# Kernel tuning notes

Hardware: AMD Instinct MI355X
Metric: run time of the kernel (lower is better)

The kernel has to match this reference:

```python
import jax, jax.numpy as jnp
import numpy as np

B, T, C, H = 512, 40, 512, 512


def _gru_dir(x, Wih, Whh, bih, bhh):
    """Single-direction PyTorch-convention GRU. x: [B,T,C] -> [B,T,H]."""
    Hh = Whh.shape[1]
    # precompute input projections for all timesteps: [B,T,3H]
    gx = jnp.einsum('btc,gc->btg', x, Wih) + bih

    def step(h, gxt):
        gh = h @ Whh.T + bhh  # [B,3H]
        r = jax.nn.sigmoid(gxt[:, :Hh] + gh[:, :Hh])
        z = jax.nn.sigmoid(gxt[:, Hh:2 * Hh] + gh[:, Hh:2 * Hh])
        n = jnp.tanh(gxt[:, 2 * Hh:] + r * gh[:, 2 * Hh:])
        h_new = (1.0 - z) * n + z * h
        return h_new, h_new

    h0 = jnp.zeros((x.shape[0], Hh), x.dtype)
    _, ys = jax.lax.scan(step, h0, jnp.swapaxes(gx, 0, 1))  # [T,B,H]
    return jnp.swapaxes(ys, 0, 1)


def setup_inputs() -> dict:
    key = jax.random.key(0)
    ks = jax.random.split(key, 10)
    s = 1.0 / np.sqrt(H)  # PyTorch default init scale
    lengths = jax.random.randint(ks[0], (B,), 5, T + 1)
    valid = jnp.arange(T)[None, :] < lengths[:, None]  # [B,T]
    ref_expr = jax.random.normal(ks[1], (B, T, C), jnp.float32) * valid[..., None]
    mk = lambda k, shape: jax.random.uniform(k, shape, jnp.float32, -s, s)
    return {
        'ref_expr': ref_expr,
        'Wih_f': mk(ks[2], (3 * H, C)), 'Whh_f': mk(ks[3], (3 * H, H)),
        'bih_f': mk(ks[4], (3 * H,)), 'bhh_f': mk(ks[5], (3 * H,)),
        'Wih_b': mk(ks[6], (3 * H, C)), 'Whh_b': mk(ks[7], (3 * H, H)),
        'bih_b': mk(ks[8], (3 * H,)), 'bhh_b': mk(ks[9], (3 * H,)),
    }


def reference(ref_expr, Wih_f, Whh_f, bih_f, bhh_f, Wih_b, Whh_b, bih_b, bhh_b):
    # padded positions are all-zero embedding vectors -> masked out
    valid = jnp.any(ref_expr != 0, axis=-1)  # [B,T], True = keep
    y_fwd = _gru_dir(ref_expr, Wih_f, Whh_f, bih_f, bhh_f)
    y_bwd = _gru_dir(ref_expr[:, ::-1], Wih_b, Whh_b, bih_b, bhh_b)[:, ::-1]
    y_word = jnp.concatenate([y_fwd, y_bwd], axis=-1)  # [B,T,2H]
    # masked max pooling over valid tokens (output_type='max')
    neg = jnp.finfo(y_word.dtype).min
    y = jnp.max(jnp.where(valid[..., None], y_word, neg), axis=1, keepdims=True)
    return y  # [B,1,2H]
```

## Files before the change

### kernel.cpp

```cpp
#include <hip/hip_runtime.h>
#include <hip/hip_bf16.h>
#include <float.h>

#define BB 512
#define TT 40
#define CC 512
#define HH 512

typedef short bf16x8 __attribute__((ext_vector_type(8)));
typedef float f32x4 __attribute__((ext_vector_type(4)));
typedef unsigned short ushortx8 __attribute__((ext_vector_type(8)));

#define LDSH 49152
#define LDSF 98304
#define LDSTOT 98320

__device__ __forceinline__ unsigned short f2bf(float f){
  union { float f; unsigned int i; } v; v.f = f;
  unsigned int r = v.i + 0x7fffu + ((v.i >> 16) & 1u);
  return (unsigned short)(r >> 16);
}

__device__ __forceinline__ bf16x8 load_sc0(const unsigned short* p){
  bf16x8 r;
  asm volatile("global_load_dwordx4 %0, %1, off sc0" : "=v"(r) : "v"(p));
  return r;
}
#define WAITV(N) do { asm volatile("s_waitcnt vmcnt(" #N ")" ::: "memory"); \
                      __builtin_amdgcn_sched_barrier(0); } while(0)

__device__ __forceinline__ float fast_sigmoid(float x){
  return __builtin_amdgcn_rcpf(1.f + __expf(-x));
}
__device__ __forceinline__ float fast_tanh(float x){
  return 1.f - 2.f*__builtin_amdgcn_rcpf(__expf(2.f*x) + 1.f);
}

__global__ void prep_x_kernel(const float* __restrict__ x, unsigned short* __restrict__ xb,
                              float* __restrict__ maskT){
  int w = blockIdx.x*4 + (threadIdx.x>>6);
  int lane = threadIdx.x & 63;
  const float* src = x + (size_t)w*CC + lane*8;
  f32x4 a = *(const f32x4*)(src);
  f32x4 b = *(const f32x4*)(src+4);
  ushortx8 o;
  o[0]=f2bf(a[0]); o[1]=f2bf(a[1]); o[2]=f2bf(a[2]); o[3]=f2bf(a[3]);
  o[4]=f2bf(b[0]); o[5]=f2bf(b[1]); o[6]=f2bf(b[2]); o[7]=f2bf(b[3]);
  *(ushortx8*)(xb + (size_t)w*CC + lane*8) = o;
  bool nz = (a[0]!=0.f)||(a[1]!=0.f)||(a[2]!=0.f)||(a[3]!=0.f)||
            (b[0]!=0.f)||(b[1]!=0.f)||(b[2]!=0.f)||(b[3]!=0.f);
  unsigned long long bal = __ballot(nz);
  if (lane==0){
    int b_ = w / TT, t_ = w % TT;
    maskT[t_*BB + b_] = bal ? 1.0f : 0.0f;
  }
}

__global__ void cvt_kernel(const float* __restrict__ src, unsigned short* __restrict__ dst, int n8){
  int i = blockIdx.x*blockDim.x + threadIdx.x;
  if (i < n8){
    f32x4 a = *(const f32x4*)(src + i*8);
    f32x4 b = *(const f32x4*)(src + i*8 + 4);
    ushortx8 o;
    o[0]=f2bf(a[0]); o[1]=f2bf(a[1]); o[2]=f2bf(a[2]); o[3]=f2bf(a[3]);
    o[4]=f2bf(b[0]); o[5]=f2bf(b[1]); o[6]=f2bf(b[2]); o[7]=f2bf(b[3]);
    *(ushortx8*)(dst + i*8) = o;
  }
}

__global__ void init_h_kernel(unsigned short* __restrict__ hb, unsigned int* __restrict__ ctr){
  int i = blockIdx.x*blockDim.x + threadIdx.x;
  hb[i] = 0;
  if (i < 8) ctr[i*32] = 0u;
}

__global__ __launch_bounds__(512, 2) void gru_persist_kernel(
    const unsigned short* __restrict__ xb,
    const unsigned short* __restrict__ wihF, const unsigned short* __restrict__ whhF,
    const unsigned short* __restrict__ wihB, const unsigned short* __restrict__ whhB,
    const float* __restrict__ bihF, const float* __restrict__ bhhF,
    const float* __restrict__ bihB, const float* __restrict__ bhhB,
    const float* __restrict__ maskT,
    unsigned short* __restrict__ hb,
    float* __restrict__ out, unsigned int* __restrict__ ctr)
{
  const int bid   = blockIdx.x;
  const int grp   = bid & 7;
  const int strip = bid >> 3;
  const int dir   = grp >> 2;
  const int bslab = grp & 3;
  const int b0 = bslab * 128;
  const int n0 = strip * 16;
  unsigned int* myctr = ctr + grp*32;

  const unsigned short* wih = dir ? wihB : wihF;
  const unsigned short* whh = dir ? whhB : whhF;
  const float* bih = dir ? bihB : bihF;
  const float* bhh = dir ? bhhB : bhhF;

  const int tid  = threadIdx.x;
  const int lane = tid & 63;
  const int lr   = lane & 15;
  const int lkg  = lane >> 4;
  const int wv   = tid >> 6;
  const int wrow = wv * 16;

  __shared__ __align__(16) char smem[LDSTOT];
  unsigned int* arrive = (unsigned int*)(smem + LDSF);

  for (int q = tid; q < 6144; q += 512) {
    const int p_  = q >= 3072;
    const int r_  = p_ ? (q - 3072) : q;
    const int row = r_ >> 6;
    const int kc  = (r_ & 63) * 8;
    const unsigned short* src =
        (p_ ? whh : wih) + ((size_t)((row>>4)*HH + n0 + (row&15)))*512 + kc;
    *(ushortx8*)(smem + p_*LDSH + row*1024 + ((kc*2) ^ ((row&15)<<4))) =
        *(const ushortx8*)src;
  }
  if (tid == 0) arrive[0] = 0u;
  __syncthreads();

  const int jj = n0 + lr;
  const float br  = bih[jj]        + bhh[jj];
  const float bz  = bih[HH + jj]   + bhh[HH + jj];
  const float bnx = bih[2*HH + jj];
  const float bnh = bhh[2*HH + jj];

  float omax[4], hreg[4];
  #pragma unroll
  for (int j=0; j<4; ++j){ omax[j] = -FLT_MAX; hreg[j] = 0.f; }

  const int swz = lr << 4;
  const char* wbx = smem + lr*1024;
  const char* wbh = smem + LDSH + lr*1024;

  for (int t = 0; t < TT; ++t) {
    const int tx = dir ? (TT-1-t) : t;
    const int bi = t & 1;
    const unsigned short* hbin = hb + (size_t)(dir*2 + bi)      * (BB*HH);
    unsigned short* hbout      = hb + (size_t)(dir*2 + (bi^1))  * (BB*HH);

    f32x4 ar = 0.f, az = 0.f, anx = 0.f, anh = 0.f;

    const unsigned short* xr0 = xb + ((size_t)(b0 + wrow + lr)*TT + tx)*CC;

    #pragma unroll
    for (int kk = 0; kk < 16; ++kk) {
      const int ko = kk*32 + lkg*8;
      bf16x8 a0 = *(const bf16x8*)(xr0 + ko);
      const int kbx = (ko*2) ^ swz;
      bf16x8 brf = *(const bf16x8*)(wbx +         kbx);
      bf16x8 bzf = *(const bf16x8*)(wbx + 16384 + kbx);
      bf16x8 bnf = *(const bf16x8*)(wbx + 32768 + kbx);
      ar  = __builtin_amdgcn_mfma_f32_16x16x32_bf16(a0, brf, ar,0,0,0);
      az  = __builtin_amdgcn_mfma_f32_16x16x32_bf16(a0, bzf, az,0,0,0);
      anx = __builtin_amdgcn_mfma_f32_16x16x32_bf16(a0, bnf, anx,0,0,0);
    }

    const f32x4 mk = *(const f32x4*)(maskT + tx*BB + b0 + wrow + lkg*4);

    if (t > 0) {
      const unsigned int tgt = 32u*(unsigned)t;
      unsigned int spin = 0;
      while (__hip_atomic_load(myctr, __ATOMIC_RELAXED, __HIP_MEMORY_SCOPE_AGENT) < tgt
             && ++spin < (1u<<24))
        __builtin_amdgcn_s_sleep(1);
    }

    WAITV(0);

    const unsigned short* hr0 = hbin + (size_t)(b0 + wrow + lr)*HH;
    bf16x8 ph[4];
    #pragma unroll
    for (int q = 0; q < 4; ++q)
      ph[q] = load_sc0(hr0 + q*32 + lkg*8);
    #pragma unroll
    for (int kk = 0; kk < 16; ++kk) {
      const int ko = kk*32 + lkg*8;
      const int kbx = (ko*2) ^ swz;
      bf16x8 brf = *(const bf16x8*)(wbh +         kbx);
      bf16x8 bzf = *(const bf16x8*)(wbh + 16384 + kbx);
      bf16x8 bnf = *(const bf16x8*)(wbh + 32768 + kbx);
      if (kk < 13)      { WAITV(3); }
      else if (kk == 13){ WAITV(2); }
      else if (kk == 14){ WAITV(1); }
      else              { WAITV(0); }
      bf16x8 c0 = ph[kk&3];
      ar  = __builtin_amdgcn_mfma_f32_16x16x32_bf16(c0, brf, ar,0,0,0);
      az  = __builtin_amdgcn_mfma_f32_16x16x32_bf16(c0, bzf, az,0,0,0);
      anh = __builtin_amdgcn_mfma_f32_16x16x32_bf16(c0, bnf, anh,0,0,0);
      if (kk < 12)
        ph[kk&3] = load_sc0(hr0 + (kk+4)*32 + lkg*8);
    }

    #pragma unroll
    for (int j=0; j<4; ++j){
      const int b = b0 + wrow + lkg*4 + j;
      const float rg = fast_sigmoid(ar[j] + br);
      const float zg = fast_sigmoid(az[j] + bz);
      const float ng = fast_tanh(anx[j] + bnx + rg*(anh[j] + bnh));
      const float hn = (1.f - zg)*ng + zg*hreg[j];
      hreg[j] = hn;
      hbout[(size_t)b*HH + jj] = f2bf(hn);
      const float cand = (mk[j] != 0.f) ? hn : -FLT_MAX;
      omax[j] = fmaxf(omax[j], cand);
    }

    if (t < TT-1) {
      WAITV(0);
      if (lane == 0)
        __hip_atomic_fetch_add(arrive, 1u, __ATOMIC_RELEASE, __HIP_MEMORY_SCOPE_WORKGROUP);
      if (wv == 0 && lane == 0) {
        const unsigned int tgt = 8u*(unsigned)(t+1);
        unsigned int spin = 0;
        while (__hip_atomic_load(arrive, __ATOMIC_ACQUIRE, __HIP_MEMORY_SCOPE_WORKGROUP) < tgt
               && ++spin < (1u<<24))
          __builtin_amdgcn_s_sleep(1);
        __hip_atomic_fetch_add(myctr, 1u, __ATOMIC_RELAXED, __HIP_MEMORY_SCOPE_AGENT);
      }
    }
  }

  #pragma unroll
  for (int j=0; j<4; ++j){
    const int b = b0 + wrow + lkg*4 + j;
    out[(size_t)b*(2*HH) + dir*HH + jj] = omax[j];
  }
}

extern "C" void kernel_launch(void* const* d_in, const int* in_sizes, int n_in,
                              void* d_out, int out_size, void* d_ws, size_t ws_size,
                              hipStream_t stream) {
  const float* x    = (const float*)d_in[0];
  const float* WihF = (const float*)d_in[1];
  const float* WhhF = (const float*)d_in[2];
  const float* bihF = (const float*)d_in[3];
  const float* bhhF = (const float*)d_in[4];
  const float* WihB = (const float*)d_in[5];
  const float* WhhB = (const float*)d_in[6];
  const float* bihB = (const float*)d_in[7];
  const float* bhhB = (const float*)d_in[8];
  float* out = (float*)d_out;

  char* ws = (char*)d_ws;
  unsigned short* xb    = (unsigned short*)(ws);
  unsigned short* wb    = (unsigned short*)(ws + 20971520);
  unsigned short* wihFb = wb;
  unsigned short* whhFb = wb + 786432;
  unsigned short* wihBb = wb + 2*786432;
  unsigned short* whhBb = wb + 3*786432;
  float* maskT = (float*)(ws + 27262976);
  unsigned short* hb = (unsigned short*)(ws + 27344896);
  unsigned int* ctr  = (unsigned int*)(ws + 29442048);

  prep_x_kernel<<<BB*TT/4, 256, 0, stream>>>(x, xb, maskT);
  cvt_kernel<<<384, 256, 0, stream>>>(WihF, wihFb, 98304);
  cvt_kernel<<<384, 256, 0, stream>>>(WhhF, whhFb, 98304);
  cvt_kernel<<<384, 256, 0, stream>>>(WihB, wihBb, 98304);
  cvt_kernel<<<384, 256, 0, stream>>>(WhhB, whhBb, 98304);
  init_h_kernel<<<4096, 256, 0, stream>>>(hb, ctr);

  gru_persist_kernel<<<256, 512, 0, stream>>>(xb, wihFb, whhFb, wihBb, whhBb,
                                              bihF, bhhF, bihB, bhhB,
                                              maskT, hb, out, ctr);
}
```

Measured before the change: 335.8 us.

## Replace shared atomic counter with per-strip flags and prefetch all h loads

The single per-group agent-scope counter that every block incremented is replaced by per-strip flag words. Each block publishes its step with a plain store, and waiters poll all 32 flags in parallel across lanes, using a ballot to check they are all ready. The last arriving wave in a block now posts the flag directly, with no dedicated spinning wave, which removes contention on the atomic and one intra-block wait. All 16 hidden-state loads are also issued up front, with graduated vmcnt waits, instead of a 4-deep rolling prefetch. The cost is higher register pressure and more polling traffic.

```diff
diff --git a/kernel.cpp b/kernel.cpp
--- a/kernel.cpp
+++ b/kernel.cpp
@@ -28,6 +28,19 @@
 }
 #define WAITV(N) do { asm volatile("s_waitcnt vmcnt(" #N ")" ::: "memory"); \
                       __builtin_amdgcn_sched_barrier(0); } while(0)
+
+__device__ __forceinline__ void waitv_idx(int n){
+  switch(n){
+    case 0:  WAITV(0);  break;  case 1:  WAITV(1);  break;
+    case 2:  WAITV(2);  break;  case 3:  WAITV(3);  break;
+    case 4:  WAITV(4);  break;  case 5:  WAITV(5);  break;
+    case 6:  WAITV(6);  break;  case 7:  WAITV(7);  break;
+    case 8:  WAITV(8);  break;  case 9:  WAITV(9);  break;
+    case 10: WAITV(10); break;  case 11: WAITV(11); break;
+    case 12: WAITV(12); break;  case 13: WAITV(13); break;
+    case 14: WAITV(14); break;  default: WAITV(15); break;
+  }
+}
 
 __device__ __forceinline__ float fast_sigmoid(float x){
   return __builtin_amdgcn_rcpf(1.f + __expf(-x));
@@ -68,10 +81,10 @@
   }
 }
 
-__global__ void init_h_kernel(unsigned short* __restrict__ hb, unsigned int* __restrict__ ctr){
+__global__ void init_h_kernel(unsigned short* __restrict__ hb, unsigned int* __restrict__ flags){
   int i = blockIdx.x*blockDim.x + threadIdx.x;
   hb[i] = 0;
-  if (i < 8) ctr[i*32] = 0u;
+  if (i < 256) flags[i] = 0u;
 }
 
 __global__ __launch_bounds__(512, 2) void gru_persist_kernel(
@@ -82,7 +95,7 @@
     const float* __restrict__ bihB, const float* __restrict__ bhhB,
     const float* __restrict__ maskT,
     unsigned short* __restrict__ hb,
-    float* __restrict__ out, unsigned int* __restrict__ ctr)
+    float* __restrict__ out, unsigned int* __restrict__ flags)
 {
   const int bid   = blockIdx.x;
   const int grp   = bid & 7;
@@ -91,7 +104,7 @@
   const int bslab = grp & 3;
   const int b0 = bslab * 128;
   const int n0 = strip * 16;
-  unsigned int* myctr = ctr + grp*32;
+  unsigned int* fl = flags + grp*32;
 
   const unsigned short* wih = dir ? wihB : wihF;
   const unsigned short* whh = dir ? whhB : whhF;
@@ -161,19 +174,24 @@
     const f32x4 mk = *(const f32x4*)(maskT + tx*BB + b0 + wrow + lkg*4);
 
     if (t > 0) {
-      const unsigned int tgt = 32u*(unsigned)t;
+      const unsigned int tgt = (unsigned)t;
       unsigned int spin = 0;
-      while (__hip_atomic_load(myctr, __ATOMIC_RELAXED, __HIP_MEMORY_SCOPE_AGENT) < tgt
-             && ++spin < (1u<<24))
+      for (;;) {
+        unsigned int v = tgt;
+        if (lane < 32)
+          v = __hip_atomic_load(&fl[lane], __ATOMIC_RELAXED, __HIP_MEMORY_SCOPE_AGENT);
+        if (__ballot(v < tgt) == 0ull) break;
+        if (++spin >= (1u<<22)) break;
         __builtin_amdgcn_s_sleep(1);
+      }
     }
 
     WAITV(0);
 
     const unsigned short* hr0 = hbin + (size_t)(b0 + wrow + lr)*HH;
-    bf16x8 ph[4];
-    #pragma unroll
-    for (int q = 0; q < 4; ++q)
+    bf16x8 ph[16];
+    #pragma unroll
+    for (int q = 0; q < 16; ++q)
       ph[q] = load_sc0(hr0 + q*32 + lkg*8);
     #pragma unroll
     for (int kk = 0; kk < 16; ++kk) {
@@ -182,16 +200,11 @@
       bf16x8 brf = *(const bf16x8*)(wbh +         kbx);
       bf16x8 bzf = *(const bf16x8*)(wbh + 16384 + kbx);
       bf16x8 bnf = *(const bf16x8*)(wbh + 32768 + kbx);
-      if (kk < 13)      { WAITV(3); }
-      else if (kk == 13){ WAITV(2); }
-      else if (kk == 14){ WAITV(1); }
-      else              { WAITV(0); }
-      bf16x8 c0 = ph[kk&3];
+      waitv_idx(15 - kk);
+      bf16x8 c0 = ph[kk];
       ar  = __builtin_amdgcn_mfma_f32_16x16x32_bf16(c0, brf, ar,0,0,0);
       az  = __builtin_amdgcn_mfma_f32_16x16x32_bf16(c0, bzf, az,0,0,0);
       anh = __builtin_amdgcn_mfma_f32_16x16x32_bf16(c0, bnf, anh,0,0,0);
-      if (kk < 12)
-        ph[kk&3] = load_sc0(hr0 + (kk+4)*32 + lkg*8);
     }
 
     #pragma unroll
@@ -209,15 +222,12 @@
 
     if (t < TT-1) {
       WAITV(0);
-      if (lane == 0)
-        __hip_atomic_fetch_add(arrive, 1u, __ATOMIC_RELEASE, __HIP_MEMORY_SCOPE_WORKGROUP);
-      if (wv == 0 && lane == 0) {
-        const unsigned int tgt = 8u*(unsigned)(t+1);
-        unsigned int spin = 0;
-        while (__hip_atomic_load(arrive, __ATOMIC_ACQUIRE, __HIP_MEMORY_SCOPE_WORKGROUP) < tgt
-               && ++spin < (1u<<24))
-          __builtin_amdgcn_s_sleep(1);
-        __hip_atomic_fetch_add(myctr, 1u, __ATOMIC_RELAXED, __HIP_MEMORY_SCOPE_AGENT);
+      if (lane == 0) {
+        unsigned int prev =
+            __hip_atomic_fetch_add(arrive, 1u, __ATOMIC_ACQ_REL, __HIP_MEMORY_SCOPE_WORKGROUP);
+        if (prev + 1u == 8u*(unsigned)(t+1))
+          __hip_atomic_store(&fl[strip], (unsigned)(t+1),
+                             __ATOMIC_RELAXED, __HIP_MEMORY_SCOPE_AGENT);
       }
     }
   }
@@ -252,16 +262,16 @@
   unsigned short* whhBb = wb + 3*786432;
   float* maskT = (float*)(ws + 27262976);
   unsigned short* hb = (unsigned short*)(ws + 27344896);
-  unsigned int* ctr  = (unsigned int*)(ws + 29442048);
+  unsigned int* flags = (unsigned int*)(ws + 29442048);
 
   prep_x_kernel<<<BB*TT/4, 256, 0, stream>>>(x, xb, maskT);
   cvt_kernel<<<384, 256, 0, stream>>>(WihF, wihFb, 98304);
   cvt_kernel<<<384, 256, 0, stream>>>(WhhF, whhFb, 98304);
   cvt_kernel<<<384, 256, 0, stream>>>(WihB, wihBb, 98304);
   cvt_kernel<<<384, 256, 0, stream>>>(WhhB, whhBb, 98304);
-  init_h_kernel<<<4096, 256, 0, stream>>>(hb, ctr);
+  init_h_kernel<<<4096, 256, 0, stream>>>(hb, flags);
 
   gru_persist_kernel<<<256, 512, 0, stream>>>(xb, wihFb, whhFb, wihBb, whhBb,
                                               bihF, bhhF, bihB, bhhB,
-                                              maskT, hb, out, ctr);
-}
+                                              maskT, hb, out, flags);
+}
```

Result: no change. 339.2 us (+1.0%).
